# Kernel tuning notes

Measured on AMD Instinct MI355X. Metric: run time of the kernel, lower is better.

Reference implementation:

```python
import jax, jax.numpy as jnp
import numpy as np

LEAKY_SLOPE = 0.2  # PyG GATConv default negative_slope
EPS = 1e-16


def _gat_layer(h_in, src, dst, W, a_src, a_dst, b, concat):
    # h_in: [N, Fin]; src/dst: [Etot] (self-loops included); W: [Fin, H*C]
    N = h_in.shape[0]
    H, C = a_src.shape
    h = (h_in @ W).reshape(N, H, C)                       # [N,H,C]
    al_s = jnp.sum(h * a_src, axis=-1)                    # [N,H]
    al_d = jnp.sum(h * a_dst, axis=-1)                    # [N,H]
    e = jax.nn.leaky_relu(al_s[src] + al_d[dst], LEAKY_SLOPE)  # [E,H]
    emax = jax.ops.segment_max(e, dst, num_segments=N)    # segment softmax over dst
    p = jnp.exp(e - emax[dst])
    denom = jax.ops.segment_sum(p, dst, num_segments=N)
    alpha = p / (denom[dst] + EPS)                        # [E,H]
    out = jax.ops.segment_sum(h[src] * alpha[:, :, None], dst, num_segments=N)  # [N,H,C]
    out = out.reshape(N, H * C) if concat else out.mean(axis=1)
    return out + b


def setup_inputs() -> dict:
    key = jax.random.key(0)
    ks = jax.random.split(key, 16)
    N, E, Fin, Hd, Hh = 10000, 320000, 256, 128, 4

    def glorot(k, shape, fan_in):
        return jax.random.normal(k, shape, dtype=jnp.float32) * (1.0 / np.sqrt(fan_in))

    inp = {
        "x": jax.random.normal(ks[0], (N, Fin), dtype=jnp.float32),
        "edge_index": jax.random.randint(ks[1], (2, E), 0, N, dtype=jnp.int32),
        # conv1: Fin -> Hd x Hh heads, concat
        "W1": glorot(ks[2], (Fin, Hh * Hd), Fin),
        "a1_src": glorot(ks[3], (Hh, Hd), Hd),
        "a1_dst": glorot(ks[4], (Hh, Hd), Hd),
        "b1": jnp.zeros((Hh * Hd,), jnp.float32),
        # conv2: Hh*Hd -> Hd x Hh heads, concat
        "W2": glorot(ks[5], (Hh * Hd, Hh * Hd), Hh * Hd),
        "a2_src": glorot(ks[6], (Hh, Hd), Hd),
        "a2_dst": glorot(ks[7], (Hh, Hd), Hd),
        "b2": jnp.zeros((Hh * Hd,), jnp.float32),
        # conv3: Hh*Hd -> Hd, 1 head, concat=False (mean)
        "W3": glorot(ks[8], (Hh * Hd, Hd), Hh * Hd),
        "a3_src": glorot(ks[9], (1, Hd), Hd),
        "a3_dst": glorot(ks[10], (1, Hd), Hd),
        "b3": jnp.zeros((Hd,), jnp.float32),
        # classifier: Hd -> Hd//2 -> 2
        "Wc1": glorot(ks[11], (Hd, Hd // 2), Hd),
        "bc1": jnp.zeros((Hd // 2,), jnp.float32),
        "Wc2": glorot(ks[12], (Hd // 2, 2), Hd // 2),
        "bc2": jnp.zeros((2,), jnp.float32),
    }
    return inp


def reference(x, edge_index, W1, a1_src, a1_dst, b1, W2, a2_src, a2_dst, b2,
              W3, a3_src, a3_dst, b3, Wc1, bc1, Wc2, bc2):
    N = x.shape[0]
    loops = jnp.arange(N, dtype=edge_index.dtype)
    src = jnp.concatenate([edge_index[0], loops])  # PyG adds self-loops
    dst = jnp.concatenate([edge_index[1], loops])

    h = jax.nn.elu(_gat_layer(x, src, dst, W1, a1_src, a1_dst, b1, concat=True))
    h = jax.nn.elu(_gat_layer(h, src, dst, W2, a2_src, a2_dst, b2, concat=True))
    embeddings = _gat_layer(h, src, dst, W3, a3_src, a3_dst, b3, concat=False)  # [N, 128]
    out = jax.nn.relu(embeddings @ Wc1 + bc1) @ Wc2 + bc2  # [N, 2]
    return out, embeddings
```

## Files before the change

kernel.cpp:

```cpp
#include <hip/hip_runtime.h>
#include <cstddef>

#define LEAKY 0.2f
#define EPS_DEN 1e-16f

typedef short bf8_t __attribute__((ext_vector_type(8)));
typedef float f4_t __attribute__((ext_vector_type(4)));
typedef unsigned short us4_t __attribute__((ext_vector_type(4)));

__device__ __forceinline__ unsigned short f2bf(float f) {
    unsigned u = __float_as_uint(f);
    unsigned r = (u + 0x7fffu + ((u >> 16) & 1u)) >> 16;
    return (unsigned short)r;
}
__device__ __forceinline__ float bf2f(unsigned short h) {
    return __uint_as_float(((unsigned)h) << 16);
}

__global__ void hist_kernel(const int* __restrict__ dst, int* __restrict__ counts, int E) {
    int i = blockIdx.x * blockDim.x + threadIdx.x;
    if (i < E) atomicAdd(&counts[dst[i]], 1);
}

__global__ void scan1_kernel(int* __restrict__ cnt, int* __restrict__ bsum, int N) {
    __shared__ int s[256];
    int t = threadIdx.x;
    int i = blockIdx.x * 256 + t;
    int v = (i < N) ? cnt[i] : 0;
    s[t] = v;
    __syncthreads();
#pragma unroll
    for (int st = 1; st < 256; st <<= 1) {
        int add = (t >= st) ? s[t - st] : 0;
        __syncthreads();
        s[t] += add;
        __syncthreads();
    }
    if (i < N) cnt[i] = s[t] - v;
    if (t == 255) bsum[blockIdx.x] = s[255];
}

__global__ void scan2_kernel(int* __restrict__ bsum, int* __restrict__ offs, int NB, int N) {
    int t = threadIdx.x;
    int v = (t < NB) ? bsum[t] : 0;
    int inc = v;
#pragma unroll
    for (int off = 1; off < 64; off <<= 1) {
        int u = __shfl_up(inc, off);
        if (t >= off) inc += u;
    }
    if (t < NB) bsum[t] = inc - v;
    if (t == 63) offs[N] = inc;
}

__global__ void scan3_kernel(int* __restrict__ cnt, const int* __restrict__ bsum,
                             int* __restrict__ offs, int N) {
    int i = blockIdx.x * 256 + threadIdx.x;
    if (i < N) {
        int o = cnt[i] + bsum[blockIdx.x];
        offs[i] = o;
        cnt[i] = o;
    }
}

__global__ void scatter_kernel(const int* __restrict__ src, const int* __restrict__ dst,
                               int* __restrict__ cursor, int* __restrict__ csrc, int E) {
    int i = blockIdx.x * blockDim.x + threadIdx.x;
    if (i < E) {
        int d = dst[i];
        int pos = atomicAdd(&cursor[d], 1);
        csrc[pos] = src[i];
    }
}

__global__ void split_kernel(const float* __restrict__ in, unsigned short* __restrict__ hi,
                             unsigned short* __restrict__ lo, int len) {
    int i = blockIdx.x * blockDim.x + threadIdx.x;
    if (i >= len) return;
    float v = in[i];
    unsigned short h = f2bf(v);
    hi[i] = h;
    lo[i] = f2bf(v - bf2f(h));
}

__global__ void wsplit_kernel(const float* __restrict__ W, unsigned short* __restrict__ hi,
                              unsigned short* __restrict__ lo, int K, int N) {
    int idx = blockIdx.x * blockDim.x + threadIdx.x;
    if (idx >= K * N) return;
    int n = idx / K, k = idx % K;
    float v = W[(size_t)k * N + n];
    unsigned short h = f2bf(v);
    hi[idx] = h;
    lo[idx] = f2bf(v - bf2f(h));
}

__global__ __launch_bounds__(256) void mfma_gemm_kernel(
    const unsigned short* __restrict__ Ahi, const unsigned short* __restrict__ Alo,
    const unsigned short* __restrict__ BThi, const unsigned short* __restrict__ BTlo,
    float* __restrict__ C, int M, int N, int K) {
    constexpr int BK = 32;
    __shared__ __align__(16) unsigned short sA[64 * BK];
    __shared__ __align__(16) unsigned short sB[128 * BK];
    int t = threadIdx.x;
    int w = t >> 6, lane = t & 63;
    int quad = lane >> 4, low = lane & 15;
    int m0 = blockIdx.y * 64, n0 = blockIdx.x * 128;
    int wm = (w & 1) * 32, wn = (w >> 1) * 64;

    f4_t acc[2][4];
#pragma unroll
    for (int i = 0; i < 2; i++)
#pragma unroll
        for (int j = 0; j < 4; j++) acc[i][j] = (f4_t){0.f, 0.f, 0.f, 0.f};

    int srow = lane >> 2;
    int schunk = lane & 3;

    const unsigned short* Ap[3] = {Ahi, Ahi, Alo};
    const unsigned short* Bp[3] = {BThi, BTlo, BThi};

    for (int pass = 0; pass < 3; pass++) {
        const unsigned short* A = Ap[pass];
        const unsigned short* B = Bp[pass];
        for (int k0 = 0; k0 < K; k0 += BK) {
            __syncthreads();
            {
                int gm = m0 + w * 16 + srow;
                if (gm >= M) gm = M - 1;
                const void* g = (const void*)(A + (size_t)gm * K + k0 + schunk * 8);
                void* l = (void*)((char*)sA + (size_t)(w * 1024));
                __builtin_amdgcn_global_load_lds((const __attribute__((address_space(1))) void*)g,
                                                 (__attribute__((address_space(3))) void*)l, 16, 0, 0);
            }
#pragma unroll
            for (int inst = 0; inst < 2; inst++) {
                int gn = n0 + w * 32 + inst * 16 + srow;
                const void* g = (const void*)(B + (size_t)gn * K + k0 + schunk * 8);
                void* l = (void*)((char*)sB + (size_t)(w * 2048 + inst * 1024));
                __builtin_amdgcn_global_load_lds((const __attribute__((address_space(1))) void*)g,
                                                 (__attribute__((address_space(3))) void*)l, 16, 0, 0);
            }
            __syncthreads();

            bf8_t af[2], bf[4];
#pragma unroll
            for (int i = 0; i < 2; i++) {
                int row = wm + i * 16 + low;
                af[i] = *(const bf8_t*)&sA[row * BK + quad * 8];
            }
#pragma unroll
            for (int j = 0; j < 4; j++) {
                int row = wn + j * 16 + low;
                bf[j] = *(const bf8_t*)&sB[row * BK + quad * 8];
            }
#pragma unroll
            for (int i = 0; i < 2; i++)
#pragma unroll
                for (int j = 0; j < 4; j++)
                    acc[i][j] = __builtin_amdgcn_mfma_f32_16x16x32_bf16(af[i], bf[j], acc[i][j], 0, 0, 0);
        }
    }

#pragma unroll
    for (int i = 0; i < 2; i++) {
#pragma unroll
        for (int r = 0; r < 4; r++) {
            int gm = m0 + wm + i * 16 + quad * 4 + r;
            if (gm >= M) continue;
#pragma unroll
            for (int j = 0; j < 4; j++) {
                int gn = n0 + wn + j * 16 + low;
                C[(size_t)gm * N + gn] = acc[i][j][r];
            }
        }
    }
}

__global__ void al_h4_kernel(const float* __restrict__ h, const float* __restrict__ a_src,
                             const float* __restrict__ a_dst, float* __restrict__ als,
                             float* __restrict__ ald, int N) {
    int wave = threadIdx.x >> 6, lane = threadIdx.x & 63;
    int n = blockIdx.x * 4 + wave;
    if (n >= N) return;
    const float* row = h + (size_t)n * 512;
    float ps[4] = {0, 0, 0, 0}, pd[4] = {0, 0, 0, 0};
#pragma unroll
    for (int k = 0; k < 8; k++) {
        int f = k * 64 + lane;
        float v = row[f];
        ps[k >> 1] += v * a_src[f];
        pd[k >> 1] += v * a_dst[f];
    }
#pragma unroll
    for (int off = 32; off; off >>= 1) {
#pragma unroll
        for (int hd = 0; hd < 4; hd++) {
            ps[hd] += __shfl_down(ps[hd], off);
            pd[hd] += __shfl_down(pd[hd], off);
        }
    }
    if (lane == 0) {
#pragma unroll
        for (int hd = 0; hd < 4; hd++) {
            als[n * 4 + hd] = ps[hd];
            ald[n * 4 + hd] = pd[hd];
        }
    }
}

__global__ void al_h1_kernel(const float* __restrict__ h, const float* __restrict__ a_src,
                             const float* __restrict__ a_dst, float* __restrict__ als,
                             float* __restrict__ ald, int N) {
    int wave = threadIdx.x >> 6, lane = threadIdx.x & 63;
    int n = blockIdx.x * 4 + wave;
    if (n >= N) return;
    const float* row = h + (size_t)n * 128;
    float v0 = row[lane], v1 = row[lane + 64];
    float ps = v0 * a_src[lane] + v1 * a_src[lane + 64];
    float pd = v0 * a_dst[lane] + v1 * a_dst[lane + 64];
#pragma unroll
    for (int off = 32; off; off >>= 1) {
        ps += __shfl_down(ps, off);
        pd += __shfl_down(pd, off);
    }
    if (lane == 0) { als[n] = ps; ald[n] = pd; }
}

__global__ void stats_h4_kernel(const int* __restrict__ csrc, const int* __restrict__ offs,
                                const float* __restrict__ als, const float* __restrict__ ald,
                                float* __restrict__ pbuf, float* __restrict__ psf,
                                float* __restrict__ rden, int N, int E) {
    int wave = threadIdx.x >> 6, lane = threadIdx.x & 63;
    int n = blockIdx.x * 4 + wave;
    if (n >= N) return;
    int hd = lane & 3, es = lane >> 2;
    float aldn = ald[n * 4 + hd];
    float selfe = als[n * 4 + hd] + aldn;
    selfe = selfe > 0.f ? selfe : LEAKY * selfe;
    int beg = offs[n], end = offs[n + 1];
    float* pb = pbuf + (size_t)hd * E;
    float m = selfe;
    for (int base = beg; base + es < end; base += 16) {
        int idx = base + es;
        int s = csrc[idx];
        float e = als[s * 4 + hd] + aldn;
        e = e > 0.f ? e : LEAKY * e;
        pb[idx] = e;
        m = fmaxf(m, e);
    }
#pragma unroll
    for (int off = 4; off < 64; off <<= 1) m = fmaxf(m, __shfl_xor(m, off));
    float d = 0.f;
    for (int base = beg; base + es < end; base += 16) {
        int idx = base + es;
        float p = __expf(pb[idx] - m);
        pb[idx] = p;
        d += p;
    }
#pragma unroll
    for (int off = 4; off < 64; off <<= 1) d += __shfl_xor(d, off);
    float pself = __expf(selfe - m);
    float r = 1.0f / (d + pself + EPS_DEN);
    if (es == 0) {
        psf[n * 4 + hd] = pself;
        rden[n * 4 + hd] = r;
    }
}

__global__ void stats_h1_kernel(const int* __restrict__ csrc, const int* __restrict__ offs,
                                const float* __restrict__ als, const float* __restrict__ ald,
                                float* __restrict__ pbuf, float* __restrict__ psf,
                                float* __restrict__ rden, int N) {
    int wave = threadIdx.x >> 6, lane = threadIdx.x & 63;
    int n = blockIdx.x * 4 + wave;
    if (n >= N) return;
    float aldn = ald[n];
    float selfe = als[n] + aldn;
    selfe = selfe > 0.f ? selfe : LEAKY * selfe;
    int beg = offs[n], end = offs[n + 1];
    float m = selfe;
    for (int base = beg; base + lane < end; base += 64) {
        int idx = base + lane;
        int s = csrc[idx];
        float e = als[s] + aldn;
        e = e > 0.f ? e : LEAKY * e;
        pbuf[idx] = e;
        m = fmaxf(m, e);
    }
#pragma unroll
    for (int off = 1; off < 64; off <<= 1) m = fmaxf(m, __shfl_xor(m, off));
    float d = 0.f;
    for (int base = beg; base + lane < end; base += 64) {
        int idx = base + lane;
        float p = __expf(pbuf[idx] - m);
        pbuf[idx] = p;
        d += p;
    }
#pragma unroll
    for (int off = 1; off < 64; off <<= 1) d += __shfl_xor(d, off);
    float pself = __expf(selfe - m);
    float r = 1.0f / (d + pself + EPS_DEN);
    if (lane == 0) { psf[n] = pself; rden[n] = r; }
}

template <bool DO_ELU>
__global__ __launch_bounds__(64) void gat_aggregate_h4_kernel(
    const float* __restrict__ h, const float* __restrict__ pbuf,
    const float* __restrict__ psf, const float* __restrict__ rden,
    const int* __restrict__ csrc, const int* __restrict__ offs,
    const float* __restrict__ bias, unsigned short* __restrict__ ohi,
    unsigned short* __restrict__ olo, int N, int E) {
    int gid = blockIdx.x;
    int head = gid & 3;
    int n = gid >> 2;
    int lane = threadIdx.x;
    int half = lane >> 5;
    int fl = (lane & 31) * 4;
    int f0 = head * 128 + fl;
    const float* pb = pbuf + (size_t)head * E;
    f4_t acc;
    {
        float pself = (half == 0) ? psf[n * 4 + head] : 0.f;
        f4_t x = *(const f4_t*)(h + (size_t)n * 512 + f0);
        acc = pself * x;
    }
    __shared__ int sSrc[64];
    __shared__ float sP[64];
    int beg = offs[n], end = offs[n + 1];
    for (int base = beg; base < end; base += 64) {
        int len = min(64, end - base);
        __syncthreads();
        if (lane < len) {
            sSrc[lane] = csrc[base + lane];
            sP[lane] = pb[base + lane];
        }
        __syncthreads();
#pragma unroll 8
        for (int c = half; c < len; c += 2) {
            const float* srow = h + (size_t)sSrc[c] * 512;
            float p = sP[c];
            f4_t x = *(const f4_t*)(srow + f0);
            acc += p * x;
        }
    }
#pragma unroll
    for (int j = 0; j < 4; j++) acc[j] += __shfl_xor(acc[j], 32);
    float r = rden[n * 4 + head];
    f4_t b = *(const f4_t*)(bias + f0);
    us4_t hs, ls;
#pragma unroll
    for (int j = 0; j < 4; j++) {
        float o = acc[j] * r + b[j];
        if (DO_ELU) o = o > 0.f ? o : (__expf(o) - 1.0f);
        unsigned short hh = f2bf(o);
        hs[j] = hh;
        ls[j] = f2bf(o - bf2f(hh));
    }
    if (half == 0) {
        size_t idx = (size_t)n * 512 + f0;
        *(us4_t*)&ohi[idx] = hs;
        *(us4_t*)&olo[idx] = ls;
    }
}

__global__ __launch_bounds__(64) void gat_aggregate_h1_kernel(
    const float* __restrict__ h, const float* __restrict__ pbuf,
    const float* __restrict__ psf, const float* __restrict__ rden,
    const int* __restrict__ csrc, const int* __restrict__ offs,
    const float* __restrict__ bias, float* __restrict__ outp, int N) {
    int n = blockIdx.x;
    int lane = threadIdx.x;
    int half = lane >> 5;
    int f0 = (lane & 31) * 4;
    f4_t acc;
    {
        float pself = (half == 0) ? psf[n] : 0.f;
        f4_t x = *(const f4_t*)(h + (size_t)n * 128 + f0);
        acc = pself * x;
    }
    __shared__ int sSrc[64];
    __shared__ float sP[64];
    int beg = offs[n], end = offs[n + 1];
    for (int base = beg; base < end; base += 64) {
        int len = min(64, end - base);
        __syncthreads();
        if (lane < len) {
            sSrc[lane] = csrc[base + lane];
            sP[lane] = pbuf[base + lane];
        }
        __syncthreads();
#pragma unroll 8
        for (int c = half; c < len; c += 2) {
            const float* srow = h + (size_t)sSrc[c] * 128;
            float p = sP[c];
            f4_t x = *(const f4_t*)(srow + f0);
            acc += p * x;
        }
    }
#pragma unroll
    for (int j = 0; j < 4; j++) acc[j] += __shfl_xor(acc[j], 32);
    if (half == 0) {
        float r = rden[n];
        f4_t b = *(const f4_t*)(bias + f0);
        f4_t o;
#pragma unroll
        for (int j = 0; j < 4; j++) o[j] = acc[j] * r + b[j];
        *(f4_t*)&outp[(size_t)n * 128 + f0] = o;
    }
}

__global__ void classifier_kernel(const float* __restrict__ emb, const float* __restrict__ Wc1,
                                  const float* __restrict__ bc1, const float* __restrict__ Wc2,
                                  const float* __restrict__ bc2, float* __restrict__ out, int N) {
    int wave = threadIdx.x >> 6, lane = threadIdx.x & 63;
    int n = blockIdx.x * 4 + wave;
    if (n >= N) return;
    const float* row = emb + (size_t)n * 128;
    float acc = bc1[lane];
#pragma unroll 4
    for (int k = 0; k < 128; k++) acc += row[k] * Wc1[k * 64 + lane];
    acc = fmaxf(acc, 0.f);
    float o0 = acc * Wc2[lane * 2 + 0];
    float o1 = acc * Wc2[lane * 2 + 1];
#pragma unroll
    for (int off = 32; off; off >>= 1) {
        o0 += __shfl_down(o0, off);
        o1 += __shfl_down(o1, off);
    }
    if (lane == 0) {
        out[n * 2 + 0] = o0 + bc2[0];
        out[n * 2 + 1] = o1 + bc2[1];
    }
}

extern "C" void kernel_launch(void* const* d_in, const int* in_sizes, int n_in,
                              void* d_out, int out_size, void* d_ws, size_t ws_size,
                              hipStream_t stream) {
    const float* x      = (const float*)d_in[0];
    const int*   ei     = (const int*)d_in[1];
    const float* W1     = (const float*)d_in[2];
    const float* a1s    = (const float*)d_in[3];
    const float* a1d    = (const float*)d_in[4];
    const float* b1     = (const float*)d_in[5];
    const float* W2     = (const float*)d_in[6];
    const float* a2s    = (const float*)d_in[7];
    const float* a2d    = (const float*)d_in[8];
    const float* b2     = (const float*)d_in[9];
    const float* W3     = (const float*)d_in[10];
    const float* a3s    = (const float*)d_in[11];
    const float* a3d    = (const float*)d_in[12];
    const float* b3     = (const float*)d_in[13];
    const float* Wc1    = (const float*)d_in[14];
    const float* bc1    = (const float*)d_in[15];
    const float* Wc2    = (const float*)d_in[16];
    const float* bc2    = (const float*)d_in[17];

    const int N = in_sizes[0] / 256;
    const int E = in_sizes[1] / 2;
    const int F = 512;

    const int* src = ei;
    const int* dst = ei + E;

    auto align = [](size_t o) { return (o + 255) & ~(size_t)255; };
    size_t o = 0;
    size_t o_G     = o; o = align(o + (size_t)N * F * 4);
    size_t o_ahi   = o; o = align(o + (size_t)N * F * 2);
    size_t o_alo   = o; o = align(o + (size_t)N * F * 2);
    size_t o_xhi   = o; o = align(o + (size_t)N * 256 * 2);
    size_t o_xlo   = o; o = align(o + (size_t)N * 256 * 2);
    size_t o_w1h   = o; o = align(o + (size_t)512 * 256 * 2);
    size_t o_w1l   = o; o = align(o + (size_t)512 * 256 * 2);
    size_t o_w2h   = o; o = align(o + (size_t)512 * 512 * 2);
    size_t o_w2l   = o; o = align(o + (size_t)512 * 512 * 2);
    size_t o_w3h   = o; o = align(o + (size_t)128 * 512 * 2);
    size_t o_w3l   = o; o = align(o + (size_t)128 * 512 * 2);
    size_t o_als   = o; o = align(o + (size_t)N * 4 * 4);
    size_t o_ald   = o; o = align(o + (size_t)N * 4 * 4);
    size_t o_psf   = o; o = align(o + (size_t)N * 4 * 4);
    size_t o_rden  = o; o = align(o + (size_t)N * 4 * 4);
    size_t o_cnt   = o; o = align(o + (size_t)N * 4);
    size_t o_off   = o; o = align(o + (size_t)(N + 1) * 4);
    size_t o_bsum  = o; o = align(o + (size_t)64 * 4);
    size_t o_csrc  = o; o = align(o + (size_t)E * 4);
    size_t o_ebuf  = o; o = align(o + (size_t)E * 4 * 4);
    (void)ws_size;

    char* ws = (char*)d_ws;
    float* bufG  = (float*)(ws + o_G);
    unsigned short* act_hi = (unsigned short*)(ws + o_ahi);
    unsigned short* act_lo = (unsigned short*)(ws + o_alo);
    unsigned short* x_hi   = (unsigned short*)(ws + o_xhi);
    unsigned short* x_lo   = (unsigned short*)(ws + o_xlo);
    unsigned short* w1h = (unsigned short*)(ws + o_w1h);
    unsigned short* w1l = (unsigned short*)(ws + o_w1l);
    unsigned short* w2h = (unsigned short*)(ws + o_w2h);
    unsigned short* w2l = (unsigned short*)(ws + o_w2l);
    unsigned short* w3h = (unsigned short*)(ws + o_w3h);
    unsigned short* w3l = (unsigned short*)(ws + o_w3l);
    float* als  = (float*)(ws + o_als);
    float* ald  = (float*)(ws + o_ald);
    float* psf  = (float*)(ws + o_psf);
    float* rden = (float*)(ws + o_rden);
    int*   cnt  = (int*)(ws + o_cnt);
    int*   offs = (int*)(ws + o_off);
    int*   bsum = (int*)(ws + o_bsum);
    int*   csrc = (int*)(ws + o_csrc);
    float* ebuf = (float*)(ws + o_ebuf);

    float* outp = (float*)d_out;
    float* emb  = (float*)d_out + (size_t)N * 2;

    hipMemsetAsync(cnt, 0, (size_t)N * 4, stream);
    int eb = (E + 255) / 256;
    int nbs = (N + 255) / 256;
    hipLaunchKernelGGL(hist_kernel, dim3(eb), dim3(256), 0, stream, dst, cnt, E);
    hipLaunchKernelGGL(scan1_kernel, dim3(nbs), dim3(256), 0, stream, cnt, bsum, N);
    hipLaunchKernelGGL(scan2_kernel, dim3(1), dim3(64), 0, stream, bsum, offs, nbs, N);
    hipLaunchKernelGGL(scan3_kernel, dim3(nbs), dim3(256), 0, stream, cnt, bsum, offs, N);
    hipLaunchKernelGGL(scatter_kernel, dim3(eb), dim3(256), 0, stream, src, dst, cnt, csrc, E);

    hipLaunchKernelGGL(split_kernel, dim3((N * 256 + 255) / 256), dim3(256), 0, stream,
                       x, x_hi, x_lo, N * 256);
    hipLaunchKernelGGL(wsplit_kernel, dim3((256 * 512 + 255) / 256), dim3(256), 0, stream,
                       W1, w1h, w1l, 256, 512);
    hipLaunchKernelGGL(wsplit_kernel, dim3((512 * 512 + 255) / 256), dim3(256), 0, stream,
                       W2, w2h, w2l, 512, 512);
    hipLaunchKernelGGL(wsplit_kernel, dim3((512 * 128 + 255) / 256), dim3(256), 0, stream,
                       W3, w3h, w3l, 512, 128);

    int nb4 = (N + 3) / 4;
    int gy  = (N + 63) / 64;

    hipLaunchKernelGGL(mfma_gemm_kernel, dim3(512 / 128, gy), dim3(256), 0, stream,
                       x_hi, x_lo, w1h, w1l, bufG, N, 512, 256);
    hipLaunchKernelGGL(al_h4_kernel, dim3(nb4), dim3(256), 0, stream, bufG, a1s, a1d, als, ald, N);
    hipLaunchKernelGGL(stats_h4_kernel, dim3(nb4), dim3(256), 0, stream,
                       csrc, offs, als, ald, ebuf, psf, rden, N, E);
    hipLaunchKernelGGL((gat_aggregate_h4_kernel<true>), dim3(N * 4), dim3(64), 0, stream,
                       bufG, ebuf, psf, rden, csrc, offs, b1, act_hi, act_lo, N, E);

    hipLaunchKernelGGL(mfma_gemm_kernel, dim3(512 / 128, gy), dim3(256), 0, stream,
                       act_hi, act_lo, w2h, w2l, bufG, N, 512, 512);
    hipLaunchKernelGGL(al_h4_kernel, dim3(nb4), dim3(256), 0, stream, bufG, a2s, a2d, als, ald, N);
    hipLaunchKernelGGL(stats_h4_kernel, dim3(nb4), dim3(256), 0, stream,
                       csrc, offs, als, ald, ebuf, psf, rden, N, E);
    hipLaunchKernelGGL((gat_aggregate_h4_kernel<true>), dim3(N * 4), dim3(64), 0, stream,
                       bufG, ebuf, psf, rden, csrc, offs, b2, act_hi, act_lo, N, E);

    hipLaunchKernelGGL(mfma_gemm_kernel, dim3(128 / 128, gy), dim3(256), 0, stream,
                       act_hi, act_lo, w3h, w3l, bufG, N, 128, 512);
    hipLaunchKernelGGL(al_h1_kernel, dim3(nb4), dim3(256), 0, stream, bufG, a3s, a3d, als, ald, N);
    hipLaunchKernelGGL(stats_h1_kernel, dim3(nb4), dim3(256), 0, stream,
                       csrc, offs, als, ald, ebuf, psf, rden, N);
    hipLaunchKernelGGL(gat_aggregate_h1_kernel, dim3(N), dim3(64), 0, stream,
                       bufG, ebuf, psf, rden, csrc, offs, b3, emb, N);

    hipLaunchKernelGGL(classifier_kernel, dim3(nb4), dim3(256), 0, stream,
                       emb, Wc1, bc1, Wc2, bc2, outp, N);
}
```

Baseline: 397.4 us.

## Fuse softmax stats into aggregation, add 128-row GEMM tile, fuse classifier

Removes the separate stats kernels by computing the per-destination max, exp and denominator inside the aggregation kernel, with a fast path that handles nodes of degree at most 64 in a single load. This drops the pbuf/psf/rden global buffers and their round trips. The layer-3 aggregation now also runs the classifier MLP from shared memory, which removes the classifier launch and the re-read of the embeddings. A new 128x128-tile MFMA GEMM is used for the two 512-wide layers to improve data reuse, at the cost of fewer blocks and more registers.

```diff
diff --git a/kernel.cpp b/kernel.cpp
--- a/kernel.cpp
+++ b/kernel.cpp
@@ -94,7 +94,92 @@
     lo[idx] = f2bf(v - bf2f(h));
 }
 
-__global__ __launch_bounds__(256) void mfma_gemm_kernel(
+__global__ __launch_bounds__(256) void mfma_gemm128_kernel(
+    const unsigned short* __restrict__ Ahi, const unsigned short* __restrict__ Alo,
+    const unsigned short* __restrict__ BThi, const unsigned short* __restrict__ BTlo,
+    float* __restrict__ C, int M, int N, int K) {
+    constexpr int BK = 32;
+    __shared__ __align__(16) unsigned short sA[128 * BK];
+    __shared__ __align__(16) unsigned short sB[128 * BK];
+    int t = threadIdx.x;
+    int w = t >> 6, lane = t & 63;
+    int quad = lane >> 4, low = lane & 15;
+    int m0 = blockIdx.y * 128, n0 = blockIdx.x * 128;
+    int wm = (w & 1) * 64, wn = (w >> 1) * 64;
+
+    f4_t acc[4][4];
+#pragma unroll
+    for (int i = 0; i < 4; i++)
+#pragma unroll
+        for (int j = 0; j < 4; j++) acc[i][j] = (f4_t){0.f, 0.f, 0.f, 0.f};
+
+    int srow = lane >> 2;
+    int schunk = lane & 3;
+
+    const unsigned short* Ap[3] = {Ahi, Ahi, Alo};
+    const unsigned short* Bp[3] = {BThi, BTlo, BThi};
+
+    for (int pass = 0; pass < 3; pass++) {
+        const unsigned short* A = Ap[pass];
+        const unsigned short* B = Bp[pass];
+        for (int k0 = 0; k0 < K; k0 += BK) {
+            __syncthreads();
+#pragma unroll
+            for (int inst = 0; inst < 2; inst++) {
+                int r = w * 32 + inst * 16 + srow;
+                int gm = m0 + r;
+                if (gm >= M) gm = M - 1;
+                const void* g = (const void*)(A + (size_t)gm * K + k0 + schunk * 8);
+                void* l = (void*)((char*)sA + (size_t)(w * 2048 + inst * 1024));
+                __builtin_amdgcn_global_load_lds((const __attribute__((address_space(1))) void*)g,
+                                                 (__attribute__((address_space(3))) void*)l, 16, 0, 0);
+            }
+#pragma unroll
+            for (int inst = 0; inst < 2; inst++) {
+                int r = w * 32 + inst * 16 + srow;
+                int gn = n0 + r;
+                const void* g = (const void*)(B + (size_t)gn * K + k0 + schunk * 8);
+                void* l = (void*)((char*)sB + (size_t)(w * 2048 + inst * 1024));
+                __builtin_amdgcn_global_load_lds((const __attribute__((address_space(1))) void*)g,
+                                                 (__attribute__((address_space(3))) void*)l, 16, 0, 0);
+            }
+            __syncthreads();
+
+            bf8_t af[4], bf[4];
+#pragma unroll
+            for (int i = 0; i < 4; i++) {
+                int row = wm + i * 16 + low;
+                af[i] = *(const bf8_t*)&sA[row * BK + quad * 8];
+            }
+#pragma unroll
+            for (int j = 0; j < 4; j++) {
+                int row = wn + j * 16 + low;
+                bf[j] = *(const bf8_t*)&sB[row * BK + quad * 8];
+            }
+#pragma unroll
+            for (int i = 0; i < 4; i++)
+#pragma unroll
+                for (int j = 0; j < 4; j++)
+                    acc[i][j] = __builtin_amdgcn_mfma_f32_16x16x32_bf16(af[i], bf[j], acc[i][j], 0, 0, 0);
+        }
+    }
+
+#pragma unroll
+    for (int i = 0; i < 4; i++) {
+#pragma unroll
+        for (int r = 0; r < 4; r++) {
+            int gm = m0 + wm + i * 16 + quad * 4 + r;
+            if (gm >= M) continue;
+#pragma unroll
+            for (int j = 0; j < 4; j++) {
+                int gn = n0 + wn + j * 16 + low;
+                C[(size_t)gm * N + gn] = acc[i][j][r];
+            }
+        }
+    }
+}
+
+__global__ __launch_bounds__(256) void mfma_gemm64_kernel(
     const unsigned short* __restrict__ Ahi, const unsigned short* __restrict__ Alo,
     const unsigned short* __restrict__ BThi, const unsigned short* __restrict__ BTlo,
     float* __restrict__ C, int M, int N, int K) {
@@ -226,90 +311,12 @@
     if (lane == 0) { als[n] = ps; ald[n] = pd; }
 }
 
-__global__ void stats_h4_kernel(const int* __restrict__ csrc, const int* __restrict__ offs,
-                                const float* __restrict__ als, const float* __restrict__ ald,
-                                float* __restrict__ pbuf, float* __restrict__ psf,
-                                float* __restrict__ rden, int N, int E) {
-    int wave = threadIdx.x >> 6, lane = threadIdx.x & 63;
-    int n = blockIdx.x * 4 + wave;
-    if (n >= N) return;
-    int hd = lane & 3, es = lane >> 2;
-    float aldn = ald[n * 4 + hd];
-    float selfe = als[n * 4 + hd] + aldn;
-    selfe = selfe > 0.f ? selfe : LEAKY * selfe;
-    int beg = offs[n], end = offs[n + 1];
-    float* pb = pbuf + (size_t)hd * E;
-    float m = selfe;
-    for (int base = beg; base + es < end; base += 16) {
-        int idx = base + es;
-        int s = csrc[idx];
-        float e = als[s * 4 + hd] + aldn;
-        e = e > 0.f ? e : LEAKY * e;
-        pb[idx] = e;
-        m = fmaxf(m, e);
-    }
-#pragma unroll
-    for (int off = 4; off < 64; off <<= 1) m = fmaxf(m, __shfl_xor(m, off));
-    float d = 0.f;
-    for (int base = beg; base + es < end; base += 16) {
-        int idx = base + es;
-        float p = __expf(pb[idx] - m);
-        pb[idx] = p;
-        d += p;
-    }
-#pragma unroll
-    for (int off = 4; off < 64; off <<= 1) d += __shfl_xor(d, off);
-    float pself = __expf(selfe - m);
-    float r = 1.0f / (d + pself + EPS_DEN);
-    if (es == 0) {
-        psf[n * 4 + hd] = pself;
-        rden[n * 4 + hd] = r;
-    }
-}
-
-__global__ void stats_h1_kernel(const int* __restrict__ csrc, const int* __restrict__ offs,
-                                const float* __restrict__ als, const float* __restrict__ ald,
-                                float* __restrict__ pbuf, float* __restrict__ psf,
-                                float* __restrict__ rden, int N) {
-    int wave = threadIdx.x >> 6, lane = threadIdx.x & 63;
-    int n = blockIdx.x * 4 + wave;
-    if (n >= N) return;
-    float aldn = ald[n];
-    float selfe = als[n] + aldn;
-    selfe = selfe > 0.f ? selfe : LEAKY * selfe;
-    int beg = offs[n], end = offs[n + 1];
-    float m = selfe;
-    for (int base = beg; base + lane < end; base += 64) {
-        int idx = base + lane;
-        int s = csrc[idx];
-        float e = als[s] + aldn;
-        e = e > 0.f ? e : LEAKY * e;
-        pbuf[idx] = e;
-        m = fmaxf(m, e);
-    }
-#pragma unroll
-    for (int off = 1; off < 64; off <<= 1) m = fmaxf(m, __shfl_xor(m, off));
-    float d = 0.f;
-    for (int base = beg; base + lane < end; base += 64) {
-        int idx = base + lane;
-        float p = __expf(pbuf[idx] - m);
-        pbuf[idx] = p;
-        d += p;
-    }
-#pragma unroll
-    for (int off = 1; off < 64; off <<= 1) d += __shfl_xor(d, off);
-    float pself = __expf(selfe - m);
-    float r = 1.0f / (d + pself + EPS_DEN);
-    if (lane == 0) { psf[n] = pself; rden[n] = r; }
-}
-
 template <bool DO_ELU>
-__global__ __launch_bounds__(64) void gat_aggregate_h4_kernel(
-    const float* __restrict__ h, const float* __restrict__ pbuf,
-    const float* __restrict__ psf, const float* __restrict__ rden,
-    const int* __restrict__ csrc, const int* __restrict__ offs,
-    const float* __restrict__ bias, unsigned short* __restrict__ ohi,
-    unsigned short* __restrict__ olo, int N, int E) {
+__global__ __launch_bounds__(64) void gat_agg_h4_fused_kernel(
+    const float* __restrict__ h, const float* __restrict__ als,
+    const float* __restrict__ ald, const int* __restrict__ csrc,
+    const int* __restrict__ offs, const float* __restrict__ bias,
+    unsigned short* __restrict__ ohi, unsigned short* __restrict__ olo, int N) {
     int gid = blockIdx.x;
     int head = gid & 3;
     int n = gid >> 2;
@@ -317,35 +324,86 @@
     int half = lane >> 5;
     int fl = (lane & 31) * 4;
     int f0 = head * 128 + fl;
-    const float* pb = pbuf + (size_t)head * E;
-    f4_t acc;
-    {
-        float pself = (half == 0) ? psf[n * 4 + head] : 0.f;
-        f4_t x = *(const f4_t*)(h + (size_t)n * 512 + f0);
-        acc = pself * x;
-    }
+
+    float aldn = ald[n * 4 + head];
+    float selfe = als[n * 4 + head] + aldn;
+    selfe = selfe > 0.f ? selfe : LEAKY * selfe;
+
     __shared__ int sSrc[64];
     __shared__ float sP[64];
     int beg = offs[n], end = offs[n + 1];
-    for (int base = beg; base < end; base += 64) {
-        int len = min(64, end - base);
+    int deg = end - beg;
+
+    f4_t acc = (f4_t){0.f, 0.f, 0.f, 0.f};
+    float dpart = 0.f;
+    float m = selfe;
+
+    if (deg <= 64) {
+        int s = 0; float e = selfe;
+        if (lane < deg) {
+            s = csrc[beg + lane];
+            e = als[s * 4 + head] + aldn;
+            e = e > 0.f ? e : LEAKY * e;
+            sSrc[lane] = s;
+            m = e > m ? e : m;
+        }
+#pragma unroll
+        for (int off = 1; off < 64; off <<= 1) m = fmaxf(m, __shfl_xor(m, off));
+        if (lane < deg) {
+            float p = __expf(e - m);
+            sP[lane] = p;
+            dpart = p;
+        }
         __syncthreads();
-        if (lane < len) {
-            sSrc[lane] = csrc[base + lane];
-            sP[lane] = pb[base + lane];
-        }
-        __syncthreads();
-#pragma unroll 8
-        for (int c = half; c < len; c += 2) {
+        for (int c = half; c < deg; c += 2) {
             const float* srow = h + (size_t)sSrc[c] * 512;
             float p = sP[c];
             f4_t x = *(const f4_t*)(srow + f0);
             acc += p * x;
         }
+    } else {
+        for (int i = beg + lane; i < end; i += 64) {
+            int s = csrc[i];
+            float e = als[s * 4 + head] + aldn;
+            e = e > 0.f ? e : LEAKY * e;
+            m = e > m ? e : m;
+        }
+#pragma unroll
+        for (int off = 1; off < 64; off <<= 1) m = fmaxf(m, __shfl_xor(m, off));
+        for (int base = beg; base < end; base += 64) {
+            int len = min(64, end - base);
+            __syncthreads();
+            if (lane < len) {
+                int s = csrc[base + lane];
+                float e = als[s * 4 + head] + aldn;
+                e = e > 0.f ? e : LEAKY * e;
+                float p = __expf(e - m);
+                sSrc[lane] = s;
+                sP[lane] = p;
+                dpart += p;
+            }
+            __syncthreads();
+#pragma unroll 8
+            for (int c = half; c < len; c += 2) {
+                const float* srow = h + (size_t)sSrc[c] * 512;
+                float p = sP[c];
+                f4_t x = *(const f4_t*)(srow + f0);
+                acc += p * x;
+            }
+        }
+    }
+
+    float pself = __expf(selfe - m);
+    if (half == 0) {
+        f4_t x = *(const f4_t*)(h + (size_t)n * 512 + f0);
+        acc += pself * x;
     }
 #pragma unroll
     for (int j = 0; j < 4; j++) acc[j] += __shfl_xor(acc[j], 32);
-    float r = rden[n * 4 + head];
+#pragma unroll
+    for (int off = 1; off < 64; off <<= 1) dpart += __shfl_xor(dpart, off);
+    float r = 1.0f / (dpart + pself + EPS_DEN);
+
     f4_t b = *(const f4_t*)(bias + f0);
     us4_t hs, ls;
 #pragma unroll
@@ -363,73 +421,123 @@
     }
 }
 
-__global__ __launch_bounds__(64) void gat_aggregate_h1_kernel(
-    const float* __restrict__ h, const float* __restrict__ pbuf,
-    const float* __restrict__ psf, const float* __restrict__ rden,
-    const int* __restrict__ csrc, const int* __restrict__ offs,
-    const float* __restrict__ bias, float* __restrict__ outp, int N) {
+__global__ __launch_bounds__(64) void gat_agg_h1_fused_kernel(
+    const float* __restrict__ h, const float* __restrict__ als,
+    const float* __restrict__ ald, const int* __restrict__ csrc,
+    const int* __restrict__ offs, const float* __restrict__ bias,
+    const float* __restrict__ Wc1, const float* __restrict__ bc1,
+    const float* __restrict__ Wc2, const float* __restrict__ bc2,
+    float* __restrict__ emb, float* __restrict__ outp, int N) {
     int n = blockIdx.x;
     int lane = threadIdx.x;
     int half = lane >> 5;
     int f0 = (lane & 31) * 4;
-    f4_t acc;
-    {
-        float pself = (half == 0) ? psf[n] : 0.f;
-        f4_t x = *(const f4_t*)(h + (size_t)n * 128 + f0);
-        acc = pself * x;
-    }
+
+    float aldn = ald[n];
+    float selfe = als[n] + aldn;
+    selfe = selfe > 0.f ? selfe : LEAKY * selfe;
+
     __shared__ int sSrc[64];
     __shared__ float sP[64];
+    __shared__ float semb[128];
     int beg = offs[n], end = offs[n + 1];
-    for (int base = beg; base < end; base += 64) {
-        int len = min(64, end - base);
+    int deg = end - beg;
+
+    f4_t acc = (f4_t){0.f, 0.f, 0.f, 0.f};
+    float dpart = 0.f;
+    float m = selfe;
+
+    if (deg <= 64) {
+        int s = 0; float e = selfe;
+        if (lane < deg) {
+            s = csrc[beg + lane];
+            e = als[s] + aldn;
+            e = e > 0.f ? e : LEAKY * e;
+            sSrc[lane] = s;
+            m = e > m ? e : m;
+        }
+#pragma unroll
+        for (int off = 1; off < 64; off <<= 1) m = fmaxf(m, __shfl_xor(m, off));
+        if (lane < deg) {
+            float p = __expf(e - m);
+            sP[lane] = p;
+            dpart = p;
+        }
         __syncthreads();
-        if (lane < len) {
-            sSrc[lane] = csrc[base + lane];
-            sP[lane] = pbuf[base + lane];
-        }
-        __syncthreads();
-#pragma unroll 8
-        for (int c = half; c < len; c += 2) {
+        for (int c = half; c < deg; c += 2) {
             const float* srow = h + (size_t)sSrc[c] * 128;
             float p = sP[c];
             f4_t x = *(const f4_t*)(srow + f0);
             acc += p * x;
         }
+    } else {
+        for (int i = beg + lane; i < end; i += 64) {
+            int s = csrc[i];
+            float e = als[s] + aldn;
+            e = e > 0.f ? e : LEAKY * e;
+            m = e > m ? e : m;
+        }
+#pragma unroll
+        for (int off = 1; off < 64; off <<= 1) m = fmaxf(m, __shfl_xor(m, off));
+        for (int base = beg; base < end; base += 64) {
+            int len = min(64, end - base);
+            __syncthreads();
+            if (lane < len) {
+                int s = csrc[base + lane];
+                float e = als[s] + aldn;
+                e = e > 0.f ? e : LEAKY * e;
+                float p = __expf(e - m);
+                sSrc[lane] = s;
+                sP[lane] = p;
+                dpart += p;
+            }
+            __syncthreads();
+#pragma unroll 8
+            for (int c = half; c < len; c += 2) {
+                const float* srow = h + (size_t)sSrc[c] * 128;
+                float p = sP[c];
+                f4_t x = *(const f4_t*)(srow + f0);
+                acc += p * x;
+            }
+        }
+    }
+
+    float pself = __expf(selfe - m);
+    if (half == 0) {
+        f4_t x = *(const f4_t*)(h + (size_t)n * 128 + f0);
+        acc += pself * x;
     }
 #pragma unroll
     for (int j = 0; j < 4; j++) acc[j] += __shfl_xor(acc[j], 32);
+#pragma unroll
+    for (int off = 1; off < 64; off <<= 1) dpart += __shfl_xor(dpart, off);
+    float r = 1.0f / (dpart + pself + EPS_DEN);
+
+    __syncthreads();
     if (half == 0) {
-        float r = rden[n];
         f4_t b = *(const f4_t*)(bias + f0);
         f4_t o;
 #pragma unroll
         for (int j = 0; j < 4; j++) o[j] = acc[j] * r + b[j];
-        *(f4_t*)&outp[(size_t)n * 128 + f0] = o;
-    }
-}
-
-__global__ void classifier_kernel(const float* __restrict__ emb, const float* __restrict__ Wc1,
-                                  const float* __restrict__ bc1, const float* __restrict__ Wc2,
-                                  const float* __restrict__ bc2, float* __restrict__ out, int N) {
-    int wave = threadIdx.x >> 6, lane = threadIdx.x & 63;
-    int n = blockIdx.x * 4 + wave;
-    if (n >= N) return;
-    const float* row = emb + (size_t)n * 128;
-    float acc = bc1[lane];
+        *(f4_t*)&semb[f0] = o;
+        *(f4_t*)&emb[(size_t)n * 128 + f0] = o;
+    }
+    __syncthreads();
+
+    float cacc = bc1[lane];
 #pragma unroll 4
-    for (int k = 0; k < 128; k++) acc += row[k] * Wc1[k * 64 + lane];
-    acc = fmaxf(acc, 0.f);
-    float o0 = acc * Wc2[lane * 2 + 0];
-    float o1 = acc * Wc2[lane * 2 + 1];
+    for (int k = 0; k < 128; k++) cacc += semb[k] * Wc1[k * 64 + lane];
+    cacc = fmaxf(cacc, 0.f);
+    float o0 = cacc * Wc2[lane * 2 + 0];
+    float o1 = cacc * Wc2[lane * 2 + 1];
 #pragma unroll
     for (int off = 32; off; off >>= 1) {
         o0 += __shfl_down(o0, off);
         o1 += __shfl_down(o1, off);
     }
     if (lane == 0) {
-        out[n * 2 + 0] = o0 + bc2[0];
-        out[n * 2 + 1] = o1 + bc2[1];
+        outp[n * 2 + 0] = o0 + bc2[0];
+        outp[n * 2 + 1] = o1 + bc2[1];
     }
 }
 
@@ -477,13 +585,10 @@
     size_t o_w3l   = o; o = align(o + (size_t)128 * 512 * 2);
     size_t o_als   = o; o = align(o + (size_t)N * 4 * 4);
     size_t o_ald   = o; o = align(o + (size_t)N * 4 * 4);
-    size_t o_psf   = o; o = align(o + (size_t)N * 4 * 4);
-    size_t o_rden  = o; o = align(o + (size_t)N * 4 * 4);
     size_t o_cnt   = o; o = align(o + (size_t)N * 4);
     size_t o_off   = o; o = align(o + (size_t)(N + 1) * 4);
     size_t o_bsum  = o; o = align(o + (size_t)64 * 4);
     size_t o_csrc  = o; o = align(o + (size_t)E * 4);
-    size_t o_ebuf  = o; o = align(o + (size_t)E * 4 * 4);
     (void)ws_size;
 
     char* ws = (char*)d_ws;
@@ -500,13 +605,10 @@
     unsigned short* w3l = (unsigned short*)(ws + o_w3l);
     float* als  = (float*)(ws + o_als);
     float* ald  = (float*)(ws + o_ald);
-    float* psf  = (float*)(ws + o_psf);
-    float* rden = (float*)(ws + o_rden);
     int*   cnt  = (int*)(ws + o_cnt);
     int*   offs = (int*)(ws + o_off);
     int*   bsum = (int*)(ws + o_bsum);
     int*   csrc = (int*)(ws + o_csrc);
-    float* ebuf = (float*)(ws + o_ebuf);
 
     float* outp = (float*)d_out;
     float* emb  = (float*)d_out + (size_t)N * 2;
@@ -530,32 +632,24 @@
                        W3, w3h, w3l, 512, 128);
 
     int nb4 = (N + 3) / 4;
-    int gy  = (N + 63) / 64;
-
-    hipLaunchKernelGGL(mfma_gemm_kernel, dim3(512 / 128, gy), dim3(256), 0, stream,
+    int gy128 = (N + 127) / 128;
+    int gy64  = (N + 63) / 64;
+
+    hipLaunchKernelGGL(mfma_gemm128_kernel, dim3(512 / 128, gy128), dim3(256), 0, stream,
                        x_hi, x_lo, w1h, w1l, bufG, N, 512, 256);
     hipLaunchKernelGGL(al_h4_kernel, dim3(nb4), dim3(256), 0, stream, bufG, a1s, a1d, als, ald, N);
-    hipLaunchKernelGGL(stats_h4_kernel, dim3(nb4), dim3(256), 0, stream,
-                       csrc, offs, als, ald, ebuf, psf, rden, N, E);
-    hipLaunchKernelGGL((gat_aggregate_h4_kernel<true>), dim3(N * 4), dim3(64), 0, stream,
-                       bufG, ebuf, psf, rden, csrc, offs, b1, act_hi, act_lo, N, E);
-
-    hipLaunchKernelGGL(mfma_gemm_kernel, dim3(512 / 128, gy), dim3(256), 0, stream,
+    hipLaunchKernelGGL((gat_agg_h4_fused_kernel<true>), dim3(N * 4), dim3(64), 0, stream,
+                       bufG, als, ald, csrc, offs, b1, act_hi, act_lo, N);
+
+    hipLaunchKernelGGL(mfma_gemm128_kernel, dim3(512 / 128, gy128), dim3(256), 0, stream,
                        act_hi, act_lo, w2h, w2l, bufG, N, 512, 512);
     hipLaunchKernelGGL(al_h4_kernel, dim3(nb4), dim3(256), 0, stream, bufG, a2s, a2d, als, ald, N);
-    hipLaunchKernelGGL(stats_h4_kernel, dim3(nb4), dim3(256), 0, stream,
-                       csrc, offs, als, ald, ebuf, psf, rden, N, E);
-    hipLaunchKernelGGL((gat_aggregate_h4_kernel<true>), dim3(N * 4), dim3(64), 0, stream,
-                       bufG, ebuf, psf, rden, csrc, offs, b2, act_hi, act_lo, N, E);
-
-    hipLaunchKernelGGL(mfma_gemm_kernel, dim3(128 / 128, gy), dim3(256), 0, stream,
+    hipLaunchKernelGGL((gat_agg_h4_fused_kernel<true>), dim3(N * 4), dim3(64), 0, stream,
+                       bufG, als, ald, csrc, offs, b2, act_hi, act_lo, N);
+
+    hipLaunchKernelGGL(mfma_gemm64_kernel, dim3(128 / 128, gy64), dim3(256), 0, stream,
                        act_hi, act_lo, w3h, w3l, bufG, N, 128, 512);
     hipLaunchKernelGGL(al_h1_kernel, dim3(nb4), dim3(256), 0, stream, bufG, a3s, a3d, als, ald, N);
-    hipLaunchKernelGGL(stats_h1_kernel, dim3(nb4), dim3(256), 0, stream,
-                       csrc, offs, als, ald, ebuf, psf, rden, N);
-    hipLaunchKernelGGL(gat_aggregate_h1_kernel, dim3(N), dim3(64), 0, stream,
-                       bufG, ebuf, psf, rden, csrc, offs, b3, emb, N);
-
-    hipLaunchKernelGGL(classifier_kernel, dim3(nb4), dim3(256), 0, stream,
-                       emb, Wc1, bc1, Wc2, bc2, outp, N);
-}
+    hipLaunchKernelGGL(gat_agg_h1_fused_kernel, dim3(N), dim3(64), 0, stream,
+                       bufG, als, ald, csrc, offs, b3, Wc1, bc1, Wc2, bc2, emb, outp, N);
+}
```

Measured after the change: 396.3 us. Within noise of the previous version (-0.3%).
